# Performance work log

Measured on AMD Instinct MI355X. Metric: run time of the kernel, lower is better.

The kernel has to match this reference:

```python
import jax, jax.numpy as jnp
import numpy as np


def conv1x1(x, w, b):
    # x: [B,C,H,W], w: [O,C], b: [O]
    return jnp.einsum('oc,bchw->bohw', w, x) + b[None, :, None, None]


def interp_bilinear_ac(x, oh, ow):
    # bilinear resize with align_corners=True, x: [B,C,H,W] -> [B,C,oh,ow]
    B, C, H, W = x.shape
    if (H, W) == (oh, ow):
        return x
    ys = jnp.linspace(0.0, H - 1.0, oh)
    xs = jnp.linspace(0.0, W - 1.0, ow)
    y0 = jnp.clip(jnp.floor(ys).astype(jnp.int32), 0, H - 1)
    y1 = jnp.minimum(y0 + 1, H - 1)
    x0 = jnp.clip(jnp.floor(xs).astype(jnp.int32), 0, W - 1)
    x1 = jnp.minimum(x0 + 1, W - 1)
    wy = (ys - y0).astype(x.dtype)
    wx = (xs - x0).astype(x.dtype)
    top = x[:, :, y0, :] * (1 - wy)[None, None, :, None] + x[:, :, y1, :] * wy[None, None, :, None]
    out = top[:, :, :, x0] * (1 - wx)[None, None, None, :] + top[:, :, :, x1] * wx[None, None, None, :]
    return out


def non_local(x, qw, qb, kw, kb, vw, vb, ow_, ob):
    B, C, H, W = x.shape
    HW = H * W
    q = conv1x1(x, qw, qb).reshape(B, -1, HW)  # [B, Ci, HW]
    k = conv1x1(x, kw, kb).reshape(B, -1, HW)
    v = conv1x1(x, vw, vb).reshape(B, -1, HW)
    attn = jnp.einsum('bci,bcj->bij', q, k)     # [B, HW, HW]
    attn = jax.nn.softmax(attn, axis=-1)
    out = jnp.einsum('bcj,bij->bci', v, attn)   # [B, Ci, HW]
    out = out.reshape(B, -1, H, W)
    return conv1x1(out, ow_, ob)


def _forward(x1, x2, x3, x4, qw, qb, kw, kb, vw, vb, ow_, ob, g1w, g1b, g2w, g2b):
    H1, W1 = x1.shape[2], x1.shape[3]
    x2_up = interp_bilinear_ac(x2, H1, W1)
    x3_up = interp_bilinear_ac(x3, H1, W1)
    x4_up = interp_bilinear_ac(x4, H1, W1)
    gf = jnp.concatenate([x1, x2_up, x3_up, x4_up], axis=1)  # [B, 128, H1, W1]
    gf = non_local(gf, qw, qb, kw, kb, vw, vb, ow_, ob)
    h = jax.nn.relu(conv1x1(gf, g1w, g1b))
    sw = jax.nn.sigmoid(conv1x1(h, g2w, g2b))                # [B, 128, H1, W1]
    w1, w2, w3, w4 = sw[:, :32], sw[:, 32:64], sw[:, 64:96], sw[:, 96:128]
    x1_out = x1 * (1 + w1)
    x2_out = x2 * (1 + interp_bilinear_ac(w2, x2.shape[2], x2.shape[3]))
    x3_out = x3 * (1 + interp_bilinear_ac(w3, x3.shape[2], x3.shape[3]))
    x4_out = x4 * (1 + interp_bilinear_ac(w4, x4.shape[2], x4.shape[3]))
    return (x1_out, x2_out, x3_out, x4_out)


def setup_inputs() -> dict:
    key = jax.random.key(0)
    ks = jax.random.split(key, 16)
    C = 128  # channel*4
    Ci = 64  # inter_channel
    Cg = 32
    d = {
        'x1': jax.random.normal(ks[0], (8, 32, 64, 64), jnp.float32),
        'x2': jax.random.normal(ks[1], (8, 32, 32, 32), jnp.float32),
        'x3': jax.random.normal(ks[2], (8, 32, 16, 16), jnp.float32),
        'x4': jax.random.normal(ks[3], (8, 32, 8, 8), jnp.float32),
        'qw': jax.random.normal(ks[4], (Ci, C), jnp.float32) * 0.05,
        'qb': jnp.zeros((Ci,), jnp.float32),
        'kw': jax.random.normal(ks[5], (Ci, C), jnp.float32) * 0.05,
        'kb': jnp.zeros((Ci,), jnp.float32),
        'vw': jax.random.normal(ks[6], (Ci, C), jnp.float32) * 0.05,
        'vb': jnp.zeros((Ci,), jnp.float32),
        'ow_': jax.random.normal(ks[7], (C, Ci), jnp.float32) * 0.05,
        'ob': jnp.zeros((C,), jnp.float32),
        'g1w': jax.random.normal(ks[8], (Cg, C), jnp.float32) * 0.05,
        'g1b': jnp.zeros((Cg,), jnp.float32),
        'g2w': jax.random.normal(ks[9], (C, Cg), jnp.float32) * 0.05,
        'g2b': jnp.zeros((C,), jnp.float32),
    }
    return d


def reference(x1, x2, x3, x4, qw, qb, kw, kb, vw, vb, ow_, ob, g1w, g1b, g2w, g2b):
    return _forward(x1, x2, x3, x4, qw, qb, kw, kb, vw, vb, ow_, ob, g1w, g1b, g2w, g2b)
```

## Files before the change

### kernel.cpp

```cpp
#include <hip/hip_runtime.h>
#include <hip/hip_bf16.h>


typedef __attribute__((ext_vector_type(8))) short s16x8;
typedef __attribute__((ext_vector_type(4))) float f32x4;

#define LOG2E 1.44269504088896340736f

__device__ __forceinline__ unsigned int f2bf(float f) {
    unsigned int u = __float_as_uint(f);
    u += 0x7fffu + ((u >> 16) & 1u);
    return u >> 16;
}
__device__ __forceinline__ unsigned int pk2bf(float a, float b) {
    union { __hip_bfloat162 h; unsigned int u; } cv;
    cv.h = __float22bfloat162_rn(make_float2(a, b));
    return cv.u;
}
__device__ __forceinline__ float bf2f(unsigned short u) {
    return __uint_as_float((unsigned int)u << 16);
}

__global__ __launch_bounds__(256) void k_prep(
    const float* __restrict__ qw, const float* __restrict__ qb,
    const float* __restrict__ kw, const float* __restrict__ kb,
    const float* __restrict__ vw, const float* __restrict__ vb,
    const float* __restrict__ ow, const float* __restrict__ g1w,
    const float* __restrict__ g2w,
    unsigned short* __restrict__ WTb, float* __restrict__ bqkv,
    unsigned short* __restrict__ owb, unsigned short* __restrict__ g1wb,
    unsigned short* __restrict__ g2wb) {
  int t = blockIdx.x * 256 + threadIdx.x;
  if (t < 192 * 128) {
    int oc = t >> 7, c = t & 127;
    float v;
    if (oc < 64)       v = qw[oc * 128 + c] * LOG2E;
    else if (oc < 128) v = kw[(oc - 64) * 128 + c];
    else               v = vw[(oc - 128) * 128 + c];
    WTb[t] = (unsigned short)f2bf(v);
  }
  if (t < 192) {
    float v;
    if (t < 64)       v = qb[t] * LOG2E;
    else if (t < 128) v = kb[t - 64];
    else              v = vb[t - 128];
    bqkv[t] = v;
  }
  if (t < 128 * 64) g1wb[t & 4095] = (unsigned short)f2bf(g1w[t & 4095]);
  if (t < 128 * 64) owb[t] = (unsigned short)f2bf(ow[t]);
  if (t < 128 * 32) g2wb[t] = (unsigned short)f2bf(g2w[t]);
}

__global__ __launch_bounds__(256) void k_qkv(
    const float* __restrict__ x1, const float* __restrict__ x2,
    const float* __restrict__ x3, const float* __restrict__ x4,
    const unsigned short* __restrict__ WTb, const float* __restrict__ bqkv,
    unsigned short* __restrict__ Qg, unsigned short* __restrict__ Kg,
    unsigned short* __restrict__ Vg) {
  __shared__ __align__(16) unsigned short gfb[128 * 136];
  unsigned int* gfbu = (unsigned int*)gfb;

  const int b = blockIdx.x >> 5;
  const int i0 = (blockIdx.x & 31) << 7;
  const int t = threadIdx.x;

  {
    const int cp = t >> 2, q = t & 3;
    const int c0 = cp << 1;
    const int pbase = q << 5;
    const int oy = (i0 >> 6) + (q >> 1);
    const int ox0 = (q & 1) << 5;

    if (cp < 16) {
      const float* s0 = x1 + (((b * 32 + c0) << 12) + (oy << 6) + ox0);
      const float* s1 = s0 + 4096;
      #pragma unroll
      for (int k8 = 0; k8 < 8; k8++) {
        float4 va = ((const float4*)s0)[k8];
        float4 vb = ((const float4*)s1)[k8];
        int p = pbase + k8 * 4;
        gfbu[(p + 0) * 68 + cp] = pk2bf(va.x, vb.x);
        gfbu[(p + 1) * 68 + cp] = pk2bf(va.y, vb.y);
        gfbu[(p + 2) * 68 + cp] = pk2bf(va.z, vb.z);
        gfbu[(p + 3) * 68 + cp] = pk2bf(va.w, vb.w);
      }
    } else {
      const float* base; int S, cs;
      if (cp < 32)      { base = x2; S = 32; cs = c0 - 32; }
      else if (cp < 48) { base = x3; S = 16; cs = c0 - 64; }
      else              { base = x4; S = 8;  cs = c0 - 96; }
      const float* pl0 = base + (b * 32 + cs) * S * S;
      const float* pl1 = pl0 + S * S;
      float yf = (float)oy * (float)(S - 1) * (1.0f / 63.0f);
      int y0 = (int)yf; if (y0 > S - 1) y0 = S - 1;
      int y1 = y0 + 1;  if (y1 > S - 1) y1 = S - 1;
      float wy = yf - (float)y0;
      const float* r00 = pl0 + y0 * S; const float* r01 = pl0 + y1 * S;
      const float* r10 = pl1 + y0 * S; const float* r11 = pl1 + y1 * S;
      for (int k = 0; k < 32; k++) {
        int ox = ox0 + k;
        float xf = (float)ox * (float)(S - 1) * (1.0f / 63.0f);
        int xx0 = (int)xf; if (xx0 > S - 1) xx0 = S - 1;
        int xx1 = xx0 + 1; if (xx1 > S - 1) xx1 = S - 1;
        float wx = xf - (float)xx0;
        float a0 = r00[xx0] + wx * (r00[xx1] - r00[xx0]);
        float b0 = r01[xx0] + wx * (r01[xx1] - r01[xx0]);
        float v0 = a0 + wy * (b0 - a0);
        float a1 = r10[xx0] + wx * (r10[xx1] - r10[xx0]);
        float b1 = r11[xx0] + wx * (r11[xx1] - r11[xx0]);
        float v1 = a1 + wy * (b1 - a1);
        gfbu[(pbase + k) * 68 + cp] = pk2bf(v0, v1);
      }
    }
  }
  __syncthreads();

  const int wv = t >> 6, lane = t & 63;
  const int r = lane & 15, qd = lane >> 4;
  const int ocb = wv * 48;

  s16x8 af[3][4];
  #pragma unroll
  for (int mti = 0; mti < 3; mti++)
    #pragma unroll
    for (int ks = 0; ks < 4; ks++)
      af[mti][ks] = *(const s16x8*)&WTb[(ocb + mti * 16 + r) * 128 + ks * 32 + qd * 8];
  float4 bias[3];
  #pragma unroll
  for (int mti = 0; mti < 3; mti++)
    bias[mti] = *(const float4*)&bqkv[ocb + mti * 16 + qd * 4];

  f32x4 zf = {0.f, 0.f, 0.f, 0.f};
  #pragma unroll 1
  for (int nt = 0; nt < 8; nt++) {
    s16x8 bfr[4];
    #pragma unroll
    for (int ks = 0; ks < 4; ks++)
      bfr[ks] = *(const s16x8*)&gfb[(nt * 16 + r) * 136 + ks * 32 + qd * 8];
    f32x4 acc[3] = {zf, zf, zf};
    #pragma unroll
    for (int ks = 0; ks < 4; ks++)
      #pragma unroll
      for (int mti = 0; mti < 3; mti++)
        acc[mti] = __builtin_amdgcn_mfma_f32_16x16x32_bf16(af[mti][ks], bfr[ks], acc[mti], 0, 0, 0);

    const int pos = i0 + nt * 16 + r;
    #pragma unroll
    for (int mti = 0; mti < 3; mti++) {
      const int gmt = wv * 3 + mti;
      float ax = acc[mti].x + bias[mti].x;
      float ay = acc[mti].y + bias[mti].y;
      float az = acc[mti].z + bias[mti].z;
      float aw = acc[mti].w + bias[mti].w;
      if (gmt < 4) {
        uint2 w; w.x = pk2bf(ax, ay); w.y = pk2bf(az, aw);
        *(uint2*)&Qg[(((b << 12) + pos) << 6) + gmt * 16 + qd * 4] = w;
      } else if (gmt < 8) {
        uint2 w; w.x = pk2bf(ax, ay); w.y = pk2bf(az, aw);
        *(uint2*)&Kg[(((b << 12) + pos) << 6) + (gmt - 4) * 16 + qd * 4] = w;
      } else {
        int ocv = (gmt - 8) * 16 + qd * 4;
        Vg[((b * 64 + ocv + 0) << 12) + pos] = (unsigned short)f2bf(ax);
        Vg[((b * 64 + ocv + 1) << 12) + pos] = (unsigned short)f2bf(ay);
        Vg[((b * 64 + ocv + 2) << 12) + pos] = (unsigned short)f2bf(az);
        Vg[((b * 64 + ocv + 3) << 12) + pos] = (unsigned short)f2bf(aw);
      }
    }
  }
}

__global__ __launch_bounds__(256, 4) void k_attn(
    const unsigned short* __restrict__ Qg, const unsigned short* __restrict__ Kg,
    const unsigned short* __restrict__ Vg, unsigned short* __restrict__ Op,
    float* __restrict__ Lp) {
  __shared__ __align__(16) unsigned short Kl[64 * 72];
  __shared__ __align__(16) unsigned short Vl[64 * 72];
  __shared__ __align__(16) unsigned short Pl[4][32 * 72];

  const int b = blockIdx.x >> 7;
  const int part = (blockIdx.x >> 5) & 3;
  const int qg = blockIdx.x & 31;
  const int i0 = qg << 7;
  const int t = threadIdx.x;
  const int wv = t >> 6, lane = t & 63;
  const int r = lane & 15, qd = lane >> 4;
  const int qbase = i0 + wv * 32;

  s16x8 qf[2][2];
  #pragma unroll
  for (int nt = 0; nt < 2; nt++)
    #pragma unroll
    for (int ks = 0; ks < 2; ks++)
      qf[nt][ks] = *(const s16x8*)&Qg[(((b << 12) + qbase + nt * 16 + r) << 6) + ks * 32 + qd * 8];

  f32x4 zf = {0.f, 0.f, 0.f, 0.f};
  f32x4 acc[2][4];
  #pragma unroll
  for (int nt = 0; nt < 2; nt++)
    #pragma unroll
    for (int mt = 0; mt < 4; mt++) acc[nt][mt] = zf;
  float l[2] = {0.f, 0.f};

  const int srow = t >> 3, sseg = t & 7;
  const unsigned short* kt0 = &Kg[(((b << 12) + (part << 10) + srow) << 6) + sseg * 8];
  const unsigned short* vt0 = &Vg[((b * 64 + srow) << 12) + (part << 10) + sseg * 8];
  uint4 pk0 = *(const uint4*)(kt0);
  uint4 pk1 = *(const uint4*)(kt0 + (32 << 6));
  uint4 pv0 = *(const uint4*)(vt0);
  uint4 pv1 = *(const uint4*)(vt0 + (32 << 12));

  for (int it = 0; it < 16; it++) {
    __syncthreads();
    *(uint4*)&Kl[srow * 72 + sseg * 8] = pk0;
    *(uint4*)&Kl[(srow + 32) * 72 + sseg * 8] = pk1;
    *(uint4*)&Vl[srow * 72 + sseg * 8] = pv0;
    *(uint4*)&Vl[(srow + 32) * 72 + sseg * 8] = pv1;
    __syncthreads();
    if (it < 15) {
      int j0 = (it + 1) << 6;
      pk0 = *(const uint4*)(kt0 + (j0 << 6));
      pk1 = *(const uint4*)(kt0 + ((j0 + 32) << 6));
      pv0 = *(const uint4*)(vt0 + j0);
      pv1 = *(const uint4*)(vt0 + (32 << 12) + j0);
    }

    f32x4 st[4][2];
    #pragma unroll
    for (int mt = 0; mt < 4; mt++) {
      s16x8 kf0 = *(const s16x8*)&Kl[(mt * 16 + r) * 72 + qd * 8];
      s16x8 kf1 = *(const s16x8*)&Kl[(mt * 16 + r) * 72 + 32 + qd * 8];
      #pragma unroll
      for (int nt = 0; nt < 2; nt++) {
        f32x4 s = __builtin_amdgcn_mfma_f32_16x16x32_bf16(kf0, qf[nt][0], zf, 0, 0, 0);
        s = __builtin_amdgcn_mfma_f32_16x16x32_bf16(kf1, qf[nt][1], s, 0, 0, 0);
        st[mt][nt] = s;
      }
    }

    #pragma unroll
    for (int nt = 0; nt < 2; nt++) {
      float rs = 0.f;
      #pragma unroll
      for (int mt = 0; mt < 4; mt++) {
        float px = exp2f(fminf(st[mt][nt].x, 80.f));
        float py = exp2f(fminf(st[mt][nt].y, 80.f));
        float pz = exp2f(fminf(st[mt][nt].z, 80.f));
        float pw = exp2f(fminf(st[mt][nt].w, 80.f));
        rs += (px + py) + (pz + pw);
        uint2 w;
        w.x = pk2bf(px, py);
        w.y = pk2bf(pz, pw);
        *(uint2*)&Pl[wv][(nt * 16 + r) * 72 + mt * 16 + qd * 4] = w;
      }
      rs += __shfl_xor(rs, 16);
      rs += __shfl_xor(rs, 32);
      l[nt] += rs;
    }
    __builtin_amdgcn_wave_barrier();

    #pragma unroll
    for (int ks = 0; ks < 2; ks++) {
      s16x8 pf0 = *(const s16x8*)&Pl[wv][(r) * 72 + ks * 32 + qd * 8];
      s16x8 pf1 = *(const s16x8*)&Pl[wv][(16 + r) * 72 + ks * 32 + qd * 8];
      #pragma unroll
      for (int mt = 0; mt < 4; mt++) {
        s16x8 vf = *(const s16x8*)&Vl[(mt * 16 + r) * 72 + ks * 32 + qd * 8];
        acc[0][mt] = __builtin_amdgcn_mfma_f32_16x16x32_bf16(vf, pf0, acc[0][mt], 0, 0, 0);
        acc[1][mt] = __builtin_amdgcn_mfma_f32_16x16x32_bf16(vf, pf1, acc[1][mt], 0, 0, 0);
      }
    }
  }

  #pragma unroll
  for (int nt = 0; nt < 2; nt++) {
    float inv = 1.0f / l[nt];
    int qrow = qbase + nt * 16 + r;
    unsigned short* orow = &Op[(((part * 8 + b) << 12) + qrow) << 6];
    #pragma unroll
    for (int mt = 0; mt < 4; mt++) {
      uint2 w;
      w.x = pk2bf(acc[nt][mt].x * inv, acc[nt][mt].y * inv);
      w.y = pk2bf(acc[nt][mt].z * inv, acc[nt][mt].w * inv);
      *(uint2*)&orow[mt * 16 + qd * 4] = w;
    }
    if (qd == 0) Lp[((part * 8 + b) << 12) + qrow] = l[nt];
  }
}

__global__ __launch_bounds__(256) void k_out(
    const unsigned short* __restrict__ Op, const float* __restrict__ Lp,
    const unsigned short* __restrict__ owb, const float* __restrict__ obias,
    const unsigned short* __restrict__ g1wb, const float* __restrict__ g1b,
    const unsigned short* __restrict__ g2wb, const float* __restrict__ g2b,
    unsigned short* __restrict__ SWb) {
  __shared__ __align__(16) unsigned short Ot[128 * 72];
  __shared__ __align__(16) unsigned short gf2t[128 * 136];
  __shared__ __align__(16) unsigned short ht[128 * 40];
  const int b = blockIdx.x >> 5;
  const int i0 = (blockIdx.x & 31) << 7;
  const int t = threadIdx.x;

  {
    const int pos = t >> 1, half = t & 1;
    const int i = i0 + pos;
    float lp4[4], lsum = 0.f;
    #pragma unroll
    for (int p = 0; p < 4; p++) { lp4[p] = Lp[((p * 8 + b) << 12) + i]; lsum += lp4[p]; }
    float o[32];
    #pragma unroll
    for (int k = 0; k < 32; k++) o[k] = 0.f;
    #pragma unroll
    for (int p = 0; p < 4; p++) {
      float w = lp4[p] / lsum;
      const uint2* prow = (const uint2*)&Op[((((p * 8 + b) << 12) + i) << 6) + half * 32];
      #pragma unroll
      for (int k = 0; k < 8; k++) {
        uint2 u = prow[k];
        o[k * 4 + 0] += w * __uint_as_float(u.x << 16);
        o[k * 4 + 1] += w * __uint_as_float(u.x & 0xFFFF0000u);
        o[k * 4 + 2] += w * __uint_as_float(u.y << 16);
        o[k * 4 + 3] += w * __uint_as_float(u.y & 0xFFFF0000u);
      }
    }
    unsigned int* dst = (unsigned int*)&Ot[pos * 72 + half * 32];
    #pragma unroll
    for (int k = 0; k < 16; k++) dst[k] = pk2bf(o[2 * k], o[2 * k + 1]);
  }
  __syncthreads();

  const int wv = t >> 6, lane = t & 63;
  const int r = lane & 15, qd = lane >> 4;
  f32x4 zf = {0.f, 0.f, 0.f, 0.f};

  {
    const int ocb = wv * 32;
    s16x8 af[2][2];
    #pragma unroll
    for (int mt = 0; mt < 2; mt++)
      #pragma unroll
      for (int ks = 0; ks < 2; ks++)
        af[mt][ks] = *(const s16x8*)&owb[(ocb + mt * 16 + r) * 64 + ks * 32 + qd * 8];
    float4 bias[2];
    #pragma unroll
    for (int mt = 0; mt < 2; mt++)
      bias[mt] = *(const float4*)&obias[ocb + mt * 16 + qd * 4];
    #pragma unroll 1
    for (int nt = 0; nt < 8; nt++) {
      s16x8 bfr[2];
      #pragma unroll
      for (int ks = 0; ks < 2; ks++)
        bfr[ks] = *(const s16x8*)&Ot[(nt * 16 + r) * 72 + ks * 32 + qd * 8];
      f32x4 acc[2] = {zf, zf};
      #pragma unroll
      for (int ks = 0; ks < 2; ks++)
        #pragma unroll
        for (int mt = 0; mt < 2; mt++)
          acc[mt] = __builtin_amdgcn_mfma_f32_16x16x32_bf16(af[mt][ks], bfr[ks], acc[mt], 0, 0, 0);
      #pragma unroll
      for (int mt = 0; mt < 2; mt++) {
        uint2 w;
        w.x = pk2bf(acc[mt].x + bias[mt].x, acc[mt].y + bias[mt].y);
        w.y = pk2bf(acc[mt].z + bias[mt].z, acc[mt].w + bias[mt].w);
        *(uint2*)&gf2t[(nt * 16 + r) * 136 + ocb + mt * 16 + qd * 4] = w;
      }
    }
  }
  __syncthreads();

  {
    s16x8 af[2][4];
    #pragma unroll
    for (int mt = 0; mt < 2; mt++)
      #pragma unroll
      for (int ks = 0; ks < 4; ks++)
        af[mt][ks] = *(const s16x8*)&g1wb[(mt * 16 + r) * 128 + ks * 32 + qd * 8];
    float4 bias[2];
    #pragma unroll
    for (int mt = 0; mt < 2; mt++)
      bias[mt] = *(const float4*)&g1b[mt * 16 + qd * 4];
    #pragma unroll
    for (int nt = 0; nt < 2; nt++) {
      const int pn = (wv * 2 + nt) * 16 + r;
      s16x8 bfr[4];
      #pragma unroll
      for (int ks = 0; ks < 4; ks++)
        bfr[ks] = *(const s16x8*)&gf2t[pn * 136 + ks * 32 + qd * 8];
      f32x4 acc[2] = {zf, zf};
      #pragma unroll
      for (int ks = 0; ks < 4; ks++)
        #pragma unroll
        for (int mt = 0; mt < 2; mt++)
          acc[mt] = __builtin_amdgcn_mfma_f32_16x16x32_bf16(af[mt][ks], bfr[ks], acc[mt], 0, 0, 0);
      #pragma unroll
      for (int mt = 0; mt < 2; mt++) {
        uint2 w;
        w.x = pk2bf(fmaxf(acc[mt].x + bias[mt].x, 0.f), fmaxf(acc[mt].y + bias[mt].y, 0.f));
        w.y = pk2bf(fmaxf(acc[mt].z + bias[mt].z, 0.f), fmaxf(acc[mt].w + bias[mt].w, 0.f));
        *(uint2*)&ht[pn * 40 + mt * 16 + qd * 4] = w;
      }
    }
  }
  __syncthreads();

  {
    const int nb = wv * 32;
    s16x8 bfg[2];
    float bias[2];
    #pragma unroll
    for (int ntl = 0; ntl < 2; ntl++) {
      bfg[ntl] = *(const s16x8*)&g2wb[(nb + ntl * 16 + r) * 32 + qd * 8];
      bias[ntl] = g2b[nb + ntl * 16 + r];
    }
    #pragma unroll 1
    for (int mt = 0; mt < 8; mt++) {
      s16x8 af = *(const s16x8*)&ht[(mt * 16 + r) * 40 + qd * 8];
      #pragma unroll
      for (int ntl = 0; ntl < 2; ntl++) {
        f32x4 acc = __builtin_amdgcn_mfma_f32_16x16x32_bf16(af, bfg[ntl], zf, 0, 0, 0);
        const int oc3 = nb + ntl * 16 + r;
        float s0 = 1.0f / (1.0f + exp2f(-LOG2E * (acc.x + bias[ntl])));
        float s1 = 1.0f / (1.0f + exp2f(-LOG2E * (acc.y + bias[ntl])));
        float s2 = 1.0f / (1.0f + exp2f(-LOG2E * (acc.z + bias[ntl])));
        float s3 = 1.0f / (1.0f + exp2f(-LOG2E * (acc.w + bias[ntl])));
        uint2 w; w.x = pk2bf(s0, s1); w.y = pk2bf(s2, s3);
        *(uint2*)&SWb[((b * 128 + oc3) << 12) + i0 + mt * 16 + qd * 4] = w;
      }
    }
  }
}

__device__ __forceinline__ float bilin64(const unsigned short* __restrict__ p,
                                         int oy, int ox, int n) {
  float yf = (float)oy * 63.0f / (float)n;
  int y0 = (int)yf; if (y0 > 63) y0 = 63;
  int y1 = y0 + 1;  if (y1 > 63) y1 = 63;
  float wy = yf - (float)y0;
  float xf = (float)ox * 63.0f / (float)n;
  int x0 = (int)xf; if (x0 > 63) x0 = 63;
  int x1 = x0 + 1;  if (x1 > 63) x1 = 63;
  float wx = xf - (float)x0;
  float v00 = bf2f(p[y0 * 64 + x0]), v01 = bf2f(p[y0 * 64 + x1]);
  float v10 = bf2f(p[y1 * 64 + x0]), v11 = bf2f(p[y1 * 64 + x1]);
  float top = v00 + wx * (v01 - v00);
  float bot = v10 + wx * (v11 - v10);
  return top + wy * (bot - top);
}

__global__ __launch_bounds__(256) void k_final(
    const float* __restrict__ x1, const float* __restrict__ x2,
    const float* __restrict__ x3, const float* __restrict__ x4,
    const unsigned short* __restrict__ SWb, float* __restrict__ out) {
  const int N1 = 1048576, N2 = 262144, N3 = 65536, N4 = 16384;
  int idx = blockIdx.x * 256 + threadIdx.x;
  if (idx < N1) {
    int b = idx >> 17, rr = idx & 131071;
    int c = rr >> 12, hw = rr & 4095;
    out[idx] = x1[idx] * (1.f + bf2f(SWb[((b * 128 + c) << 12) + hw]));
  } else if (idx < N1 + N2) {
    int i2 = idx - N1;
    int b = i2 >> 15, rr = i2 & 32767;
    int c = rr >> 10, oy = (rr >> 5) & 31, ox = rr & 31;
    float w = bilin64(SWb + ((b * 128 + 32 + c) << 12), oy, ox, 31);
    out[idx] = x2[i2] * (1.f + w);
  } else if (idx < N1 + N2 + N3) {
    int i3 = idx - N1 - N2;
    int b = i3 >> 13, rr = i3 & 8191;
    int c = rr >> 8, oy = (rr >> 4) & 15, ox = rr & 15;
    float w = bilin64(SWb + ((b * 128 + 64 + c) << 12), oy, ox, 15);
    out[idx] = x3[i3] * (1.f + w);
  } else if (idx < N1 + N2 + N3 + N4) {
    int i4 = idx - N1 - N2 - N3;
    int b = i4 >> 11, rr = i4 & 2047;
    int c = rr >> 6, oy = (rr >> 3) & 7, ox = rr & 7;
    float w = bilin64(SWb + ((b * 128 + 96 + c) << 12), oy, ox, 7);
    out[idx] = x4[i4] * (1.f + w);
  }
}

extern "C" void kernel_launch(void* const* d_in, const int* in_sizes, int n_in,
                              void* d_out, int out_size, void* d_ws, size_t ws_size,
                              hipStream_t stream) {
  const float* x1  = (const float*)d_in[0];
  const float* x2  = (const float*)d_in[1];
  const float* x3  = (const float*)d_in[2];
  const float* x4  = (const float*)d_in[3];
  const float* qw  = (const float*)d_in[4];
  const float* qb  = (const float*)d_in[5];
  const float* kw  = (const float*)d_in[6];
  const float* kb  = (const float*)d_in[7];
  const float* vw  = (const float*)d_in[8];
  const float* vb  = (const float*)d_in[9];
  const float* ow  = (const float*)d_in[10];
  const float* ob  = (const float*)d_in[11];
  const float* g1w = (const float*)d_in[12];
  const float* g1b = (const float*)d_in[13];
  const float* g2w = (const float*)d_in[14];
  const float* g2b = (const float*)d_in[15];
  float* out = (float*)d_out;

  char* ws = (char*)d_ws;
  unsigned short* Qg  = (unsigned short*)(ws + 0);
  unsigned short* Kg  = (unsigned short*)(ws + 4194304);
  unsigned short* Vg  = (unsigned short*)(ws + 8388608);
  unsigned short* SWb = (unsigned short*)(ws + 0);
  unsigned short* Op  = (unsigned short*)(ws + 12582912);
  float* Lp   = (float*)(ws + 29360128);
  unsigned short* WTb = (unsigned short*)(ws + 29884416);
  float* bqkv = (float*)(ws + 29933568);
  unsigned short* owb  = (unsigned short*)(ws + 29934592);
  unsigned short* g1wb = (unsigned short*)(ws + 29950976);
  unsigned short* g2wb = (unsigned short*)(ws + 29959168);

  k_prep<<<96, 256, 0, stream>>>(qw, qb, kw, kb, vw, vb, ow, g1w, g2w,
                                 WTb, bqkv, owb, g1wb, g2wb);
  k_qkv<<<256, 256, 0, stream>>>(x1, x2, x3, x4, WTb, bqkv, Qg, Kg, Vg);
  k_attn<<<1024, 256, 0, stream>>>(Qg, Kg, Vg, Op, Lp);
  k_out<<<256, 256, 0, stream>>>(Op, Lp, owb, ob, g1wb, g1b, g2wb, g2b, SWb);
  k_final<<<5440, 256, 0, stream>>>(x1, x2, x3, x4, SWb, out);
}
```

Measured before the change: 201.7 us.

## Double per-wave query tile in attention and halve QKV projection tile

The attention kernel now gives each wave 64 query rows instead of 32, so each staged K/V tile in shared memory is reused across twice as many queries. Grid size halves to 512 blocks and the occupancy hint drops from 4 to 2 blocks per CU to allow the larger register accumulators. Softmax exponentiation now happens right after each score MFMA instead of in a separate pass. Separately, the QKV projection kernel processes 64 positions per block instead of 128, doubling its grid to 512 blocks for better parallelism. The trade-off is higher register and LDS pressure and lower occupancy in the attention kernel.

Result: slower. 208.3 us (+3.3%).

```diff
diff --git a/kernel.cpp b/kernel.cpp
--- a/kernel.cpp
+++ b/kernel.cpp
@@ -57,28 +57,28 @@
     const unsigned short* __restrict__ WTb, const float* __restrict__ bqkv,
     unsigned short* __restrict__ Qg, unsigned short* __restrict__ Kg,
     unsigned short* __restrict__ Vg) {
-  __shared__ __align__(16) unsigned short gfb[128 * 136];
+  __shared__ __align__(16) unsigned short gfb[64 * 136];
   unsigned int* gfbu = (unsigned int*)gfb;
 
-  const int b = blockIdx.x >> 5;
-  const int i0 = (blockIdx.x & 31) << 7;
+  const int b = blockIdx.x >> 6;
+  const int i0 = (blockIdx.x & 63) << 6;
   const int t = threadIdx.x;
 
   {
     const int cp = t >> 2, q = t & 3;
     const int c0 = cp << 1;
-    const int pbase = q << 5;
-    const int oy = (i0 >> 6) + (q >> 1);
-    const int ox0 = (q & 1) << 5;
+    const int pbase = q << 4;
+    const int oy = i0 >> 6;
+    const int ox0 = pbase;
 
     if (cp < 16) {
       const float* s0 = x1 + (((b * 32 + c0) << 12) + (oy << 6) + ox0);
       const float* s1 = s0 + 4096;
       #pragma unroll
-      for (int k8 = 0; k8 < 8; k8++) {
-        float4 va = ((const float4*)s0)[k8];
-        float4 vb = ((const float4*)s1)[k8];
-        int p = pbase + k8 * 4;
+      for (int k4 = 0; k4 < 4; k4++) {
+        float4 va = ((const float4*)s0)[k4];
+        float4 vb = ((const float4*)s1)[k4];
+        int p = pbase + k4 * 4;
         gfbu[(p + 0) * 68 + cp] = pk2bf(va.x, vb.x);
         gfbu[(p + 1) * 68 + cp] = pk2bf(va.y, vb.y);
         gfbu[(p + 2) * 68 + cp] = pk2bf(va.z, vb.z);
@@ -97,7 +97,7 @@
       float wy = yf - (float)y0;
       const float* r00 = pl0 + y0 * S; const float* r01 = pl0 + y1 * S;
       const float* r10 = pl1 + y0 * S; const float* r11 = pl1 + y1 * S;
-      for (int k = 0; k < 32; k++) {
+      for (int k = 0; k < 16; k++) {
         int ox = ox0 + k;
         float xf = (float)ox * (float)(S - 1) * (1.0f / 63.0f);
         int xx0 = (int)xf; if (xx0 > S - 1) xx0 = S - 1;
@@ -132,7 +132,7 @@
 
   f32x4 zf = {0.f, 0.f, 0.f, 0.f};
   #pragma unroll 1
-  for (int nt = 0; nt < 8; nt++) {
+  for (int nt = 0; nt < 4; nt++) {
     s16x8 bfr[4];
     #pragma unroll
     for (int ks = 0; ks < 4; ks++)
@@ -169,37 +169,37 @@
   }
 }
 
-__global__ __launch_bounds__(256, 4) void k_attn(
+__global__ __launch_bounds__(256, 2) void k_attn(
     const unsigned short* __restrict__ Qg, const unsigned short* __restrict__ Kg,
     const unsigned short* __restrict__ Vg, unsigned short* __restrict__ Op,
     float* __restrict__ Lp) {
   __shared__ __align__(16) unsigned short Kl[64 * 72];
   __shared__ __align__(16) unsigned short Vl[64 * 72];
-  __shared__ __align__(16) unsigned short Pl[4][32 * 72];
-
-  const int b = blockIdx.x >> 7;
-  const int part = (blockIdx.x >> 5) & 3;
-  const int qg = blockIdx.x & 31;
-  const int i0 = qg << 7;
+  __shared__ __align__(16) unsigned short Pl[4][64 * 72];
+
+  const int b = blockIdx.x >> 6;
+  const int part = (blockIdx.x >> 4) & 3;
+  const int qg = blockIdx.x & 15;
+  const int i0 = qg << 8;
   const int t = threadIdx.x;
   const int wv = t >> 6, lane = t & 63;
   const int r = lane & 15, qd = lane >> 4;
-  const int qbase = i0 + wv * 32;
-
-  s16x8 qf[2][2];
+  const int qbase = i0 + wv * 64;
+
+  s16x8 qf[4][2];
   #pragma unroll
-  for (int nt = 0; nt < 2; nt++)
+  for (int nt = 0; nt < 4; nt++)
     #pragma unroll
     for (int ks = 0; ks < 2; ks++)
       qf[nt][ks] = *(const s16x8*)&Qg[(((b << 12) + qbase + nt * 16 + r) << 6) + ks * 32 + qd * 8];
 
   f32x4 zf = {0.f, 0.f, 0.f, 0.f};
-  f32x4 acc[2][4];
+  f32x4 acc[4][4];
   #pragma unroll
-  for (int nt = 0; nt < 2; nt++)
+  for (int nt = 0; nt < 4; nt++)
     #pragma unroll
     for (int mt = 0; mt < 4; mt++) acc[nt][mt] = zf;
-  float l[2] = {0.f, 0.f};
+  float l[4] = {0.f, 0.f, 0.f, 0.f};
 
   const int srow = t >> 3, sseg = t & 7;
   const unsigned short* kt0 = &Kg[(((b << 12) + (part << 10) + srow) << 6) + sseg * 8];
@@ -224,55 +224,53 @@
       pv1 = *(const uint4*)(vt0 + (32 << 12) + j0);
     }
 
-    f32x4 st[4][2];
+    float rs[4] = {0.f, 0.f, 0.f, 0.f};
     #pragma unroll
     for (int mt = 0; mt < 4; mt++) {
       s16x8 kf0 = *(const s16x8*)&Kl[(mt * 16 + r) * 72 + qd * 8];
       s16x8 kf1 = *(const s16x8*)&Kl[(mt * 16 + r) * 72 + 32 + qd * 8];
       #pragma unroll
-      for (int nt = 0; nt < 2; nt++) {
+      for (int nt = 0; nt < 4; nt++) {
         f32x4 s = __builtin_amdgcn_mfma_f32_16x16x32_bf16(kf0, qf[nt][0], zf, 0, 0, 0);
         s = __builtin_amdgcn_mfma_f32_16x16x32_bf16(kf1, qf[nt][1], s, 0, 0, 0);
-        st[mt][nt] = s;
-      }
-    }
-
-    #pragma unroll
-    for (int nt = 0; nt < 2; nt++) {
-      float rs = 0.f;
-      #pragma unroll
-      for (int mt = 0; mt < 4; mt++) {
-        float px = exp2f(fminf(st[mt][nt].x, 80.f));
-        float py = exp2f(fminf(st[mt][nt].y, 80.f));
-        float pz = exp2f(fminf(st[mt][nt].z, 80.f));
-        float pw = exp2f(fminf(st[mt][nt].w, 80.f));
-        rs += (px + py) + (pz + pw);
+        float px = exp2f(fminf(s.x, 80.f));
+        float py = exp2f(fminf(s.y, 80.f));
+        float pz = exp2f(fminf(s.z, 80.f));
+        float pw = exp2f(fminf(s.w, 80.f));
+        rs[nt] += (px + py) + (pz + pw);
         uint2 w;
         w.x = pk2bf(px, py);
         w.y = pk2bf(pz, pw);
         *(uint2*)&Pl[wv][(nt * 16 + r) * 72 + mt * 16 + qd * 4] = w;
       }
-      rs += __shfl_xor(rs, 16);
-      rs += __shfl_xor(rs, 32);
-      l[nt] += rs;
+    }
+    #pragma unroll
+    for (int nt = 0; nt < 4; nt++) {
+      float v = rs[nt];
+      v += __shfl_xor(v, 16);
+      v += __shfl_xor(v, 32);
+      l[nt] += v;
     }
     __builtin_amdgcn_wave_barrier();
 
     #pragma unroll
     for (int ks = 0; ks < 2; ks++) {
-      s16x8 pf0 = *(const s16x8*)&Pl[wv][(r) * 72 + ks * 32 + qd * 8];
-      s16x8 pf1 = *(const s16x8*)&Pl[wv][(16 + r) * 72 + ks * 32 + qd * 8];
-      #pragma unroll
-      for (int mt = 0; mt < 4; mt++) {
-        s16x8 vf = *(const s16x8*)&Vl[(mt * 16 + r) * 72 + ks * 32 + qd * 8];
-        acc[0][mt] = __builtin_amdgcn_mfma_f32_16x16x32_bf16(vf, pf0, acc[0][mt], 0, 0, 0);
-        acc[1][mt] = __builtin_amdgcn_mfma_f32_16x16x32_bf16(vf, pf1, acc[1][mt], 0, 0, 0);
+      s16x8 vf[4];
+      #pragma unroll
+      for (int mt = 0; mt < 4; mt++)
+        vf[mt] = *(const s16x8*)&Vl[(mt * 16 + r) * 72 + ks * 32 + qd * 8];
+      #pragma unroll
+      for (int nt = 0; nt < 4; nt++) {
+        s16x8 pf = *(const s16x8*)&Pl[wv][(nt * 16 + r) * 72 + ks * 32 + qd * 8];
+        #pragma unroll
+        for (int mt = 0; mt < 4; mt++)
+          acc[nt][mt] = __builtin_amdgcn_mfma_f32_16x16x32_bf16(vf[mt], pf, acc[nt][mt], 0, 0, 0);
       }
     }
   }
 
   #pragma unroll
-  for (int nt = 0; nt < 2; nt++) {
+  for (int nt = 0; nt < 4; nt++) {
     float inv = 1.0f / l[nt];
     int qrow = qbase + nt * 16 + r;
     unsigned short* orow = &Op[(((part * 8 + b) << 12) + qrow) << 6];
@@ -513,8 +511,8 @@
 
   k_prep<<<96, 256, 0, stream>>>(qw, qb, kw, kb, vw, vb, ow, g1w, g2w,
                                  WTb, bqkv, owb, g1wb, g2wb);
-  k_qkv<<<256, 256, 0, stream>>>(x1, x2, x3, x4, WTb, bqkv, Qg, Kg, Vg);
-  k_attn<<<1024, 256, 0, stream>>>(Qg, Kg, Vg, Op, Lp);
+  k_qkv<<<512, 256, 0, stream>>>(x1, x2, x3, x4, WTb, bqkv, Qg, Kg, Vg);
+  k_attn<<<512, 256, 0, stream>>>(Qg, Kg, Vg, Op, Lp);
   k_out<<<256, 256, 0, stream>>>(Op, Lp, owb, ob, g1wb, g1b, g2wb, g2b, SWb);
   k_final<<<5440, 256, 0, stream>>>(x1, x2, x3, x4, SWb, out);
 }
```
